# Performance work log

Measured on AMD Instinct MI355X. Metric: run time of the kernel, lower is better.

Reference implementation:

```python
import jax, jax.numpy as jnp
import numpy as np

N_NODES = 50000
N_EDGES = 800000
D = 64
N_REL = 16


def setup_inputs() -> dict:
    key = jax.random.key(0)
    ks = jax.random.split(key, 8)
    return {
        "nfeat": jax.random.normal(ks[0], (N_NODES, D), dtype=jnp.float32),
        "efeat": jax.random.normal(ks[1], (N_EDGES, D), dtype=jnp.float32),
        "relation_W": jax.random.normal(ks[2], (N_REL, D, D), dtype=jnp.float32) * (1.0 / np.sqrt(D)),
        "W1": jax.random.normal(ks[3], (D, D), dtype=jnp.float32) * (1.0 / np.sqrt(D)),
        "W2": jax.random.normal(ks[4], (D, D), dtype=jnp.float32) * (1.0 / np.sqrt(D)),
        "src": jax.random.randint(ks[5], (N_EDGES,), 0, N_NODES, dtype=jnp.int32),
        "dst": jax.random.randint(ks[6], (N_EDGES,), 0, N_NODES, dtype=jnp.int32),
        "etype": jax.random.randint(ks[7], (N_EDGES,), 0, N_REL, dtype=jnp.int32),
    }


def _leaky_relu(x, slope=0.01):
    return jnp.where(x >= 0, x, slope * x)


def reference(nfeat, efeat, relation_W, W1, W2, src, dst, etype):
    N, Din = nfeat.shape
    R, _, Dr = relation_W.shape
    # W_r h for every (relation, node) pair, then gather per-edge.
    # Mathematically identical to per-edge bmm_maybe_select, but avoids the
    # (E, Din, Dr) per-edge weight materialization.
    proj = jnp.einsum('nd,rde->rne', nfeat, relation_W).reshape(R * N, Dr)  # (R*N, Dr)
    flat_src = etype * N + src
    flat_dst = etype * N + dst
    t_r = proj[flat_src]  # (E, Dr) == W_r h_t
    h_r = proj[flat_dst]  # (E, Dr) == W_r h_h
    # att = (W_r h_t)^T tanh(W_r h_h + e_r)
    att = jnp.sum(t_r * jnp.tanh(h_r + efeat), axis=-1)  # (E,)
    # edge softmax grouped by destination node
    seg_max = jax.ops.segment_max(att, dst, num_segments=N)  # (N,)
    ex = jnp.exp(att - seg_max[dst])
    denom = jax.ops.segment_sum(ex, dst, num_segments=N)  # (N,)
    a = ex / denom[dst]  # (E,)
    # u_mul_e + sum scatter aggregation
    h_neighbor = jax.ops.segment_sum(nfeat[src] * a[:, None], dst, num_segments=N)  # (N, Din)
    # Bi-interaction residual
    out = _leaky_relu((nfeat + h_neighbor) @ W1) + _leaky_relu((nfeat * h_neighbor) @ W2)
    return (h_neighbor, out)
```

## Files before the change

### kernel.cpp

```cpp
#include <hip/hip_runtime.h>
#include <math.h>


#define DIM 64
#define PA 72

typedef _Float16 half8 __attribute__((ext_vector_type(8)));
typedef float f32x4 __attribute__((ext_vector_type(4)));

__device__ __forceinline__ float4 f4zero() { return make_float4(0.f, 0.f, 0.f, 0.f); }

__device__ __forceinline__ float fast_tanh(float x) {
    float ex = __expf(2.0f * x);
    return 1.0f - 2.0f / (ex + 1.0f);
}

__global__ __launch_bounds__(256) void k_hist(const int* __restrict__ dst,
                                              int* __restrict__ deg,
                                              int* __restrict__ rank, int E) {
    int e = blockIdx.x * 256 + threadIdx.x;
    if (e < E) rank[e] = atomicAdd(&deg[dst[e]], 1);
}

__global__ __launch_bounds__(256) void k_scan1(const int* __restrict__ deg,
                                               int* __restrict__ epart,
                                               int* __restrict__ bsum, int N) {
    __shared__ int sh[256];
    int i = blockIdx.x * 256 + threadIdx.x;
    int t = threadIdx.x;
    int v = (i < N) ? deg[i] : 0;
    sh[t] = v;
    __syncthreads();
#pragma unroll
    for (int d = 1; d < 256; d <<= 1) {
        int o = (t >= d) ? sh[t - d] : 0;
        __syncthreads();
        sh[t] += o;
        __syncthreads();
    }
    if (i < N) epart[i] = sh[t] - v;
    if (t == 255) bsum[blockIdx.x] = sh[255];
}

__global__ __launch_bounds__(1024) void k_scan2(const int* __restrict__ epart,
                                                const int* __restrict__ bsum,
                                                int nb,
                                                int* __restrict__ off,
                                                int N, int E) {
    __shared__ int bx[256];
    int t = threadIdx.x;
    int v = 0;
    if (t < 256) {
        v = (t < nb) ? bsum[t] : 0;
        bx[t] = v;
    }
    __syncthreads();
#pragma unroll
    for (int d = 1; d < 256; d <<= 1) {
        int o = 0;
        if (t < 256 && t >= d) o = bx[t - d];
        __syncthreads();
        if (t < 256) bx[t] += o;
        __syncthreads();
    }
    if (t < 256) bx[t] -= v;
    __syncthreads();
    for (int i = t; i < N; i += 1024)
        off[i] = epart[i] + bx[i >> 8];
    if (t == 0) off[N] = E;
}

__global__ __launch_bounds__(256) void k_thist(const int* __restrict__ etype,
                                               int* __restrict__ bh,
                                               int nbe, int E) {
    __shared__ int h[16];
    const int tx = threadIdx.x, b = blockIdx.x;
    if (tx < 16) h[tx] = 0;
    __syncthreads();
    int e = b * 256 + tx;
    if (e < E) atomicAdd(&h[etype[e]], 1);
    __syncthreads();
    if (tx < 16) bh[(size_t)tx * nbe + b] = h[tx];
}

__global__ __launch_bounds__(1024) void k_tscan(int* __restrict__ bh, int nbe,
                                                int* __restrict__ hdr) {
    __shared__ int cntS[16];
    __shared__ int tstartS[16];
    const int tx = threadIdx.x;
    const int w = tx >> 6;
    const int lane = tx & 63;
    int* row = bh + (size_t)w * nbe;

    int run = 0;
    for (int i0 = 0; i0 < nbe; i0 += 64) {
        int idx = i0 + lane;
        int v = (idx < nbe) ? row[idx] : 0;
        int incl = v;
#pragma unroll
        for (int d = 1; d < 64; d <<= 1) {
            int o = __shfl_up(incl, d);
            if (lane >= d) incl += o;
        }
        if (idx < nbe) row[idx] = run + (incl - v);
        run += __shfl(incl, 63);
    }
    if (lane == 0) cntS[w] = run;
    __syncthreads();
    if (tx == 0) {
        int ts = 0, tp = 0;
        for (int r = 0; r < 16; ++r) {
            tstartS[r] = ts;
            hdr[r] = ts;
            hdr[17 + r] = tp;
            ts += cntS[r];
            tp += (cntS[r] + 63) >> 6;
        }
        hdr[16] = ts;
        hdr[33] = tp;
    }
    __syncthreads();
    const int t0 = tstartS[w];
    for (int i0 = 0; i0 < nbe; i0 += 64) {
        int idx = i0 + lane;
        if (idx < nbe) row[idx] += t0;
    }
}

__global__ __launch_bounds__(256) void k_tfill(const int* __restrict__ src,
                                               const int* __restrict__ dst,
                                               const int* __restrict__ etype,
                                               const int* __restrict__ rank,
                                               const int* __restrict__ off,
                                               const int* __restrict__ bh, int nbe,
                                               int* __restrict__ sS,
                                               int* __restrict__ dS,
                                               int* __restrict__ pS,
                                               int* __restrict__ eS, int E) {
    __shared__ int h[16];
    const int tx = threadIdx.x, b = blockIdx.x;
    if (tx < 16) h[tx] = 0;
    __syncthreads();
    int e = b * 256 + tx;
    if (e < E) {
        int r = etype[e];
        int mr = atomicAdd(&h[r], 1);
        int slot = bh[(size_t)r * nbe + b] + mr;
        int d = dst[e];
        sS[slot] = src[e];
        dS[slot] = d;
        pS[slot] = off[d] + rank[e];
        eS[slot] = e;
    }
}

__global__ __launch_bounds__(256) void k_attE(const float* __restrict__ nfeat,
                                              const float* __restrict__ efeat,
                                              const float* __restrict__ relW,
                                              const int* __restrict__ hdr,
                                              const int* __restrict__ sS,
                                              const int* __restrict__ dS,
                                              const int* __restrict__ pS,
                                              const int* __restrict__ eS,
                                              float* __restrict__ att_s,
                                              int* __restrict__ src_s) {
    __shared__ _Float16 shS[64 * PA];
    __shared__ _Float16 shD[64 * PA];
    __shared__ _Float16 shB[64 * PA];

    const int bid = blockIdx.x;
    if (bid >= hdr[33]) return;
    int r = 0;
    while (r < 15 && bid >= hdr[17 + r + 1]) ++r;
    const int e0 = hdr[r] + ((bid - hdr[17 + r]) << 6);
    const int cnt = min(64, hdr[r + 1] - e0);

    const int tx = threadIdx.x;

    const float4* Wr4 = (const float4*)(relW + (size_t)r * DIM * DIM);
#pragma unroll
    for (int i = 0; i < 4; ++i) {
        int idx = tx + 256 * i;
        int d = idx >> 4, c = (idx & 15) * 4;
        float4 v = Wr4[idx];
        shB[(c + 0) * PA + d] = (_Float16)v.x;
        shB[(c + 1) * PA + d] = (_Float16)v.y;
        shB[(c + 2) * PA + d] = (_Float16)v.z;
        shB[(c + 3) * PA + d] = (_Float16)v.w;
    }
#pragma unroll
    for (int i = 0; i < 4; ++i) {
        int idx = tx + 256 * i;
        int row = idx >> 4, c = idx & 15;
        bool ok = (row < cnt);
        int sn = ok ? sS[e0 + row] : 0;
        int dn = ok ? dS[e0 + row] : 0;
        float4 a = ok ? *(const float4*)&nfeat[(size_t)sn * DIM + c * 4] : f4zero();
        float4 b = ok ? *(const float4*)&nfeat[(size_t)dn * DIM + c * 4] : f4zero();
        _Float16* p1 = &shS[row * PA + c * 4];
        _Float16* p2 = &shD[row * PA + c * 4];
        p1[0] = (_Float16)a.x; p1[1] = (_Float16)a.y;
        p1[2] = (_Float16)a.z; p1[3] = (_Float16)a.w;
        p2[0] = (_Float16)b.x; p2[1] = (_Float16)b.y;
        p2[2] = (_Float16)b.z; p2[3] = (_Float16)b.w;
    }
    __syncthreads();

    const int w = tx >> 6;
    const int lane = tx & 63;
    const int lm = lane & 15;
    const int lq = lane >> 4;
    const int m0 = w * 16;

    half8 as0 = *(const half8*)&shS[(m0 + lm) * PA + 0 * 32 + lq * 8];
    half8 as1 = *(const half8*)&shS[(m0 + lm) * PA + 1 * 32 + lq * 8];
    half8 ad0 = *(const half8*)&shD[(m0 + lm) * PA + 0 * 32 + lq * 8];
    half8 ad1 = *(const half8*)&shD[(m0 + lm) * PA + 1 * 32 + lq * 8];

    f32x4 T[4], H[4];
#pragma unroll
    for (int ct = 0; ct < 4; ++ct) {
        half8 b0 = *(const half8*)&shB[(ct * 16 + lm) * PA + 0 * 32 + lq * 8];
        half8 b1 = *(const half8*)&shB[(ct * 16 + lm) * PA + 1 * 32 + lq * 8];
        f32x4 c1 = {0.f, 0.f, 0.f, 0.f};
        f32x4 c2 = {0.f, 0.f, 0.f, 0.f};
        c1 = __builtin_amdgcn_mfma_f32_16x16x32_f16(as0, b0, c1, 0, 0, 0);
        c1 = __builtin_amdgcn_mfma_f32_16x16x32_f16(as1, b1, c1, 0, 0, 0);
        c2 = __builtin_amdgcn_mfma_f32_16x16x32_f16(ad0, b0, c2, 0, 0, 0);
        c2 = __builtin_amdgcn_mfma_f32_16x16x32_f16(ad1, b1, c2, 0, 0, 0);
        T[ct] = c1;
        H[ct] = c2;
    }

    int ei[4];
#pragma unroll
    for (int i = 0; i < 4; ++i) {
        int row = m0 + lq * 4 + i;
        ei[i] = (row < cnt) ? eS[e0 + row] : -1;
    }

    float part[4] = {0.f, 0.f, 0.f, 0.f};
#pragma unroll
    for (int ct = 0; ct < 4; ++ct) {
        int col = ct * 16 + lm;
#pragma unroll
        for (int i = 0; i < 4; ++i) {
            float ef = (ei[i] >= 0)
                ? __builtin_nontemporal_load(&efeat[(size_t)ei[i] * DIM + col])
                : 0.f;
            part[i] = fmaf(T[ct][i], fast_tanh(H[ct][i] + ef), part[i]);
        }
    }
#pragma unroll
    for (int i = 0; i < 4; ++i) {
        part[i] += __shfl_xor(part[i], 1);
        part[i] += __shfl_xor(part[i], 2);
        part[i] += __shfl_xor(part[i], 4);
        part[i] += __shfl_xor(part[i], 8);
    }
    if (lm == 0) {
#pragma unroll
        for (int i = 0; i < 4; ++i) {
            int row = m0 + lq * 4 + i;
            if (row < cnt) {
                int p = pS[e0 + row];
                att_s[p] = part[i];
                src_s[p] = sS[e0 + row];
            }
        }
    }
}

__global__ __launch_bounds__(256) void k_agg(const float* __restrict__ att_s,
                                             const int* __restrict__ src_s,
                                             const float* __restrict__ nfeat,
                                             const int* __restrict__ off,
                                             float* __restrict__ hn, int N) {
    const int node = blockIdx.x * 4 + (threadIdx.x >> 6);
    if (node >= N) return;
    const int lane = threadIdx.x & 63;
    const int qw = lane >> 4;
    const int ql = lane & 15;

    const int jb = off[node];
    const int je = off[node + 1];

    float m = -INFINITY;
    for (int j0 = jb; j0 < je; j0 += 64) {
        int j = j0 + lane;
        float a = (j < je) ? att_s[j] : -INFINITY;
        m = fmaxf(m, a);
    }
#pragma unroll
    for (int ms = 32; ms; ms >>= 1) m = fmaxf(m, __shfl_xor(m, ms));

    float pl = 0.f;
    f32x4 acc = {0.f, 0.f, 0.f, 0.f};
    for (int j0 = jb; j0 < je; j0 += 64) {
        int j = j0 + lane;
        int cnt = min(64, je - j0);
        float a = (j < je) ? att_s[j] : -INFINITY;
        float p = __expf(a - m);
        int s = (j < je) ? src_s[j] : 0;
        pl += p;

        int jj = 0;
        for (; jj + 15 < cnt; jj += 16) {
            float pj[4]; int sj[4]; f32x4 x[4];
#pragma unroll
            for (int u = 0; u < 4; ++u) {
                int eidx = jj + u * 4 + qw;
                pj[u] = __shfl(p, eidx);
                sj[u] = __shfl(s, eidx);
            }
#pragma unroll
            for (int u = 0; u < 4; ++u)
                x[u] = *(const f32x4*)&nfeat[(size_t)sj[u] * DIM + ql * 4];
#pragma unroll
            for (int u = 0; u < 4; ++u) {
                acc[0] = fmaf(pj[u], x[u][0], acc[0]);
                acc[1] = fmaf(pj[u], x[u][1], acc[1]);
                acc[2] = fmaf(pj[u], x[u][2], acc[2]);
                acc[3] = fmaf(pj[u], x[u][3], acc[3]);
            }
        }
        for (; jj < cnt; jj += 4) {
            int eidx = jj + qw;
            int ec = (eidx < cnt) ? eidx : (cnt - 1);
            float pj = __shfl(p, ec);
            int sj = __shfl(s, ec);
            if (eidx < cnt) {
                f32x4 x = *(const f32x4*)&nfeat[(size_t)sj * DIM + ql * 4];
                acc[0] = fmaf(pj, x[0], acc[0]);
                acc[1] = fmaf(pj, x[1], acc[1]);
                acc[2] = fmaf(pj, x[2], acc[2]);
                acc[3] = fmaf(pj, x[3], acc[3]);
            }
        }
    }
#pragma unroll
    for (int ms = 32; ms; ms >>= 1) pl += __shfl_xor(pl, ms);

#pragma unroll
    for (int c = 0; c < 4; ++c) {
        acc[c] += __shfl_xor(acc[c], 16);
        acc[c] += __shfl_xor(acc[c], 32);
    }

    const float inv = (je > jb) ? 1.0f / pl : 0.f;
    if (qw == 0) {
        f32x4 hv = {acc[0] * inv, acc[1] * inv, acc[2] * inv, acc[3] * inv};
        *(f32x4*)&hn[(size_t)node * DIM + ql * 4] = hv;
    }
}

__global__ __launch_bounds__(256) void k_bi(const float* __restrict__ nfeat,
                                            const float* __restrict__ hn,
                                            const float* __restrict__ W1,
                                            const float* __restrict__ W2,
                                            float* __restrict__ out, int N) {
    __shared__ _Float16 shMem[4 * 64 * PA];
    _Float16* shA1 = shMem;
    _Float16* shA2 = shMem + 64 * PA;
    _Float16* shB1 = shMem + 2 * 64 * PA;
    _Float16* shB2 = shMem + 3 * 64 * PA;

    const int tx = threadIdx.x;
    const int n0 = blockIdx.x * 64;

    const float4* nf4 = (const float4*)(nfeat + (size_t)n0 * DIM);
    const float4* hn4 = (const float4*)(hn + (size_t)n0 * DIM);
#pragma unroll
    for (int i = 0; i < 4; ++i) {
        int idx = tx + 256 * i;
        int row = idx >> 4, c = idx & 15;
        bool ok = (n0 + row < N);
        float4 a = ok ? nf4[idx] : f4zero();
        float4 b = ok ? hn4[idx] : f4zero();
        _Float16* p1 = &shA1[row * PA + c * 4];
        _Float16* p2 = &shA2[row * PA + c * 4];
        p1[0] = (_Float16)(a.x + b.x); p2[0] = (_Float16)(a.x * b.x);
        p1[1] = (_Float16)(a.y + b.y); p2[1] = (_Float16)(a.y * b.y);
        p1[2] = (_Float16)(a.z + b.z); p2[2] = (_Float16)(a.z * b.z);
        p1[3] = (_Float16)(a.w + b.w); p2[3] = (_Float16)(a.w * b.w);
    }
    const float4* w14 = (const float4*)W1;
    const float4* w24 = (const float4*)W2;
#pragma unroll
    for (int i = 0; i < 4; ++i) {
        int idx = tx + 256 * i;
        int k = idx >> 4, c = (idx & 15) * 4;
        float4 v = w14[idx];
        shB1[(c + 0) * PA + k] = (_Float16)v.x;
        shB1[(c + 1) * PA + k] = (_Float16)v.y;
        shB1[(c + 2) * PA + k] = (_Float16)v.z;
        shB1[(c + 3) * PA + k] = (_Float16)v.w;
        float4 u = w24[idx];
        shB2[(c + 0) * PA + k] = (_Float16)u.x;
        shB2[(c + 1) * PA + k] = (_Float16)u.y;
        shB2[(c + 2) * PA + k] = (_Float16)u.z;
        shB2[(c + 3) * PA + k] = (_Float16)u.w;
    }
    __syncthreads();

    const int w = tx >> 6;
    const int lane = tx & 63;
    const int lm = lane & 15;
    const int lq = lane >> 4;
    const int m0 = w * 16;

    half8 a10 = *(const half8*)&shA1[(m0 + lm) * PA + 0 * 32 + lq * 8];
    half8 a11 = *(const half8*)&shA1[(m0 + lm) * PA + 1 * 32 + lq * 8];
    half8 a20 = *(const half8*)&shA2[(m0 + lm) * PA + 0 * 32 + lq * 8];
    half8 a21 = *(const half8*)&shA2[(m0 + lm) * PA + 1 * 32 + lq * 8];

    f32x4 res[4];
#pragma unroll
    for (int ct = 0; ct < 4; ++ct) {
        half8 b10 = *(const half8*)&shB1[(ct * 16 + lm) * PA + 0 * 32 + lq * 8];
        half8 b11 = *(const half8*)&shB1[(ct * 16 + lm) * PA + 1 * 32 + lq * 8];
        half8 b20 = *(const half8*)&shB2[(ct * 16 + lm) * PA + 0 * 32 + lq * 8];
        half8 b21 = *(const half8*)&shB2[(ct * 16 + lm) * PA + 1 * 32 + lq * 8];
        f32x4 c1 = {0.f, 0.f, 0.f, 0.f};
        f32x4 c2 = {0.f, 0.f, 0.f, 0.f};
        c1 = __builtin_amdgcn_mfma_f32_16x16x32_f16(a10, b10, c1, 0, 0, 0);
        c1 = __builtin_amdgcn_mfma_f32_16x16x32_f16(a11, b11, c1, 0, 0, 0);
        c2 = __builtin_amdgcn_mfma_f32_16x16x32_f16(a20, b20, c2, 0, 0, 0);
        c2 = __builtin_amdgcn_mfma_f32_16x16x32_f16(a21, b21, c2, 0, 0, 0);
#pragma unroll
        for (int i = 0; i < 4; ++i) {
            float o1 = c1[i], o2 = c2[i];
            res[ct][i] = (o1 >= 0.f ? o1 : 0.01f * o1) + (o2 >= 0.f ? o2 : 0.01f * o2);
        }
    }

    __syncthreads();
    float* shSt = (float*)shMem;
#pragma unroll
    for (int ct = 0; ct < 4; ++ct)
#pragma unroll
        for (int i = 0; i < 4; ++i)
            shSt[(m0 + lq * 4 + i) * 68 + ct * 16 + lm] = res[ct][i];
    __syncthreads();

    float* outp = out + (size_t)n0 * DIM;
#pragma unroll
    for (int k = 0; k < 4; ++k) {
        int idx = tx + 256 * k;
        int row = idx >> 4, cc = idx & 15;
        if (n0 + row < N) {
            float4 v = *(const float4*)&shSt[row * 68 + cc * 4];
            *(float4*)&outp[(size_t)row * DIM + cc * 4] = v;
        }
    }
}

extern "C" void kernel_launch(void* const* d_in, const int* in_sizes, int n_in,
                              void* d_out, int out_size, void* d_ws, size_t ws_size,
                              hipStream_t stream) {
    const float* nfeat = (const float*)d_in[0];
    const float* efeat = (const float*)d_in[1];
    const float* relW  = (const float*)d_in[2];
    const float* W1    = (const float*)d_in[3];
    const float* W2    = (const float*)d_in[4];
    const int* src   = (const int*)d_in[5];
    const int* dst   = (const int*)d_in[6];
    const int* etype = (const int*)d_in[7];

    const int N = in_sizes[0] / DIM;
    const int E = in_sizes[5];
    const int NB = (N + 255) / 256;
    const int NBE = (E + 255) / 256;

    float* out = (float*)d_out;
    float* hn  = out;
    float* bi  = out + (size_t)N * DIM;

    int* deg    = (int*)d_ws;
    int* off    = deg + N;
    int* epart  = off + (N + 1);
    int* bsum   = epart + N;
    int* rank   = bsum + 256;
    int* src_s  = rank + E;
    float* att_s = (float*)(src_s + E);
    int* bh     = (int*)(att_s + E);
    int* hdr    = bh + (size_t)16 * NBE;
    int* sS     = hdr + 64;
    int* dS     = sS + E;
    int* pS     = dS + E;
    int* eS     = pS + E;

    (void)hipMemsetAsync(deg, 0, (size_t)N * sizeof(int), stream);

    k_hist<<<NBE, 256, 0, stream>>>(dst, deg, rank, E);
    k_scan1<<<NB, 256, 0, stream>>>(deg, epart, bsum, N);
    k_scan2<<<1, 1024, 0, stream>>>(epart, bsum, NB, off, N, E);

    k_thist<<<NBE, 256, 0, stream>>>(etype, bh, NBE, E);
    k_tscan<<<1, 1024, 0, stream>>>(bh, NBE, hdr);
    k_tfill<<<NBE, 256, 0, stream>>>(src, dst, etype, rank, off, bh, NBE,
                                     sS, dS, pS, eS, E);

    const int nTiles = (E + 63) / 64 + 16;
    k_attE<<<nTiles, 256, 0, stream>>>(nfeat, efeat, relW, hdr,
                                       sS, dS, pS, eS, att_s, src_s);

    k_agg<<<(N + 3) / 4, 256, 0, stream>>>(att_s, src_s, nfeat, off, hn, N);

    k_bi<<<(N + 63) / 64, 256, 0, stream>>>(nfeat, hn, W1, W2, bi, N);
}
```

Measured before the change: 548.4 us.

## Fuse preprocessing kernels, pretranspose relation weights, stage efeat rows through LDS

Merges the degree histogram and the per-block etype histogram into one kernel, which also converts the relation weights once into a transposed fp16 buffer. The two single-block scans are merged into one launch. The attention kernel now reads the prepared fp16 weights straight into registers instead of rebuilding them in LDS in every tile. It also loads efeat rows coalesced into shared memory as float4 instead of scattered scalar loads per MFMA output. This removes two launches and redundant per-tile weight conversion, at the cost of extra syncs and LDS reuse in the attention kernel.

```diff
diff --git a/kernel.cpp b/kernel.cpp
--- a/kernel.cpp
+++ b/kernel.cpp
@@ -6,6 +6,7 @@
 #define PA 72
 
 typedef _Float16 half8 __attribute__((ext_vector_type(8)));
+typedef _Float16 half4 __attribute__((ext_vector_type(4)));
 typedef float f32x4 __attribute__((ext_vector_type(4)));
 
 __device__ __forceinline__ float4 f4zero() { return make_float4(0.f, 0.f, 0.f, 0.f); }
@@ -15,11 +16,40 @@
     return 1.0f - 2.0f / (ex + 1.0f);
 }
 
-__global__ __launch_bounds__(256) void k_hist(const int* __restrict__ dst,
-                                              int* __restrict__ deg,
-                                              int* __restrict__ rank, int E) {
-    int e = blockIdx.x * 256 + threadIdx.x;
-    if (e < E) rank[e] = atomicAdd(&deg[dst[e]], 1);
+__global__ __launch_bounds__(256) void k_histT(const int* __restrict__ dst,
+                                               const int* __restrict__ etype,
+                                               const float* __restrict__ relW,
+                                               int* __restrict__ deg,
+                                               int* __restrict__ rank,
+                                               int* __restrict__ bh,
+                                               _Float16* __restrict__ WT,
+                                               int nbe, int E) {
+    __shared__ int h[16];
+    const int tx = threadIdx.x, b = blockIdx.x;
+    if (tx < 16) h[tx] = 0;
+    __syncthreads();
+    int e = b * 256 + tx;
+    if (e < E) {
+        rank[e] = atomicAdd(&deg[dst[e]], 1);
+        atomicAdd(&h[etype[e]], 1);
+    }
+    __syncthreads();
+    if (tx < 16) bh[(size_t)tx * nbe + b] = h[tx];
+
+    if (b < 16) {
+        const float4* Wr4 = (const float4*)(relW + (size_t)b * DIM * DIM);
+        _Float16* wt = WT + (size_t)b * DIM * DIM;
+#pragma unroll
+        for (int i = 0; i < 4; ++i) {
+            int idx = tx + 256 * i;
+            int k = idx >> 4, c4 = (idx & 15) * 4;
+            float4 v = Wr4[idx];
+            wt[(c4 + 0) * DIM + k] = (_Float16)v.x;
+            wt[(c4 + 1) * DIM + k] = (_Float16)v.y;
+            wt[(c4 + 2) * DIM + k] = (_Float16)v.z;
+            wt[(c4 + 3) * DIM + k] = (_Float16)v.w;
+        }
+    }
 }
 
 __global__ __launch_bounds__(256) void k_scan1(const int* __restrict__ deg,
@@ -42,70 +72,37 @@
     if (t == 255) bsum[blockIdx.x] = sh[255];
 }
 
-__global__ __launch_bounds__(1024) void k_scan2(const int* __restrict__ epart,
+__global__ __launch_bounds__(1024) void k_scanF(int* __restrict__ bh, int nbe,
+                                                int* __restrict__ hdr,
+                                                const int* __restrict__ epart,
                                                 const int* __restrict__ bsum,
                                                 int nb,
                                                 int* __restrict__ off,
                                                 int N, int E) {
-    __shared__ int bx[256];
-    int t = threadIdx.x;
-    int v = 0;
-    if (t < 256) {
-        v = (t < nb) ? bsum[t] : 0;
-        bx[t] = v;
-    }
-    __syncthreads();
-#pragma unroll
-    for (int d = 1; d < 256; d <<= 1) {
-        int o = 0;
-        if (t < 256 && t >= d) o = bx[t - d];
-        __syncthreads();
-        if (t < 256) bx[t] += o;
-        __syncthreads();
-    }
-    if (t < 256) bx[t] -= v;
-    __syncthreads();
-    for (int i = t; i < N; i += 1024)
-        off[i] = epart[i] + bx[i >> 8];
-    if (t == 0) off[N] = E;
-}
-
-__global__ __launch_bounds__(256) void k_thist(const int* __restrict__ etype,
-                                               int* __restrict__ bh,
-                                               int nbe, int E) {
-    __shared__ int h[16];
-    const int tx = threadIdx.x, b = blockIdx.x;
-    if (tx < 16) h[tx] = 0;
-    __syncthreads();
-    int e = b * 256 + tx;
-    if (e < E) atomicAdd(&h[etype[e]], 1);
-    __syncthreads();
-    if (tx < 16) bh[(size_t)tx * nbe + b] = h[tx];
-}
-
-__global__ __launch_bounds__(1024) void k_tscan(int* __restrict__ bh, int nbe,
-                                                int* __restrict__ hdr) {
     __shared__ int cntS[16];
     __shared__ int tstartS[16];
+    __shared__ int bx[256];
     const int tx = threadIdx.x;
     const int w = tx >> 6;
     const int lane = tx & 63;
-    int* row = bh + (size_t)w * nbe;
-
-    int run = 0;
-    for (int i0 = 0; i0 < nbe; i0 += 64) {
-        int idx = i0 + lane;
-        int v = (idx < nbe) ? row[idx] : 0;
-        int incl = v;
-#pragma unroll
-        for (int d = 1; d < 64; d <<= 1) {
-            int o = __shfl_up(incl, d);
-            if (lane >= d) incl += o;
-        }
-        if (idx < nbe) row[idx] = run + (incl - v);
-        run += __shfl(incl, 63);
-    }
-    if (lane == 0) cntS[w] = run;
+
+    {
+        int* row = bh + (size_t)w * nbe;
+        int run = 0;
+        for (int i0 = 0; i0 < nbe; i0 += 64) {
+            int idx = i0 + lane;
+            int v = (idx < nbe) ? row[idx] : 0;
+            int incl = v;
+#pragma unroll
+            for (int d = 1; d < 64; d <<= 1) {
+                int o = __shfl_up(incl, d);
+                if (lane >= d) incl += o;
+            }
+            if (idx < nbe) row[idx] = run + (incl - v);
+            run += __shfl(incl, 63);
+        }
+        if (lane == 0) cntS[w] = run;
+    }
     __syncthreads();
     if (tx == 0) {
         int ts = 0, tp = 0;
@@ -120,11 +117,33 @@
         hdr[33] = tp;
     }
     __syncthreads();
-    const int t0 = tstartS[w];
-    for (int i0 = 0; i0 < nbe; i0 += 64) {
-        int idx = i0 + lane;
-        if (idx < nbe) row[idx] += t0;
-    }
+    {
+        const int t0 = tstartS[w];
+        int* row = bh + (size_t)w * nbe;
+        for (int i0 = 0; i0 < nbe; i0 += 64) {
+            int idx = i0 + lane;
+            if (idx < nbe) row[idx] += t0;
+        }
+    }
+    int v = 0;
+    if (tx < 256) {
+        v = (tx < nb) ? bsum[tx] : 0;
+        bx[tx] = v;
+    }
+    __syncthreads();
+#pragma unroll
+    for (int d = 1; d < 256; d <<= 1) {
+        int o = 0;
+        if (tx < 256 && tx >= d) o = bx[tx - d];
+        __syncthreads();
+        if (tx < 256) bx[tx] += o;
+        __syncthreads();
+    }
+    if (tx < 256) bx[tx] -= v;
+    __syncthreads();
+    for (int i = tx; i < N; i += 1024)
+        off[i] = epart[i] + bx[i >> 8];
+    if (tx == 0) off[N] = E;
 }
 
 __global__ __launch_bounds__(256) void k_tfill(const int* __restrict__ src,
@@ -156,7 +175,7 @@
 
 __global__ __launch_bounds__(256) void k_attE(const float* __restrict__ nfeat,
                                               const float* __restrict__ efeat,
-                                              const float* __restrict__ relW,
+                                              const _Float16* __restrict__ WT,
                                               const int* __restrict__ hdr,
                                               const int* __restrict__ sS,
                                               const int* __restrict__ dS,
@@ -164,9 +183,9 @@
                                               const int* __restrict__ eS,
                                               float* __restrict__ att_s,
                                               int* __restrict__ src_s) {
-    __shared__ _Float16 shS[64 * PA];
-    __shared__ _Float16 shD[64 * PA];
-    __shared__ _Float16 shB[64 * PA];
+    __shared__ _Float16 shMem[2 * 64 * PA];
+    _Float16* shS = shMem;
+    _Float16* shD = shMem + 64 * PA;
 
     const int bid = blockIdx.x;
     if (bid >= hdr[33]) return;
@@ -174,20 +193,8 @@
     while (r < 15 && bid >= hdr[17 + r + 1]) ++r;
     const int e0 = hdr[r] + ((bid - hdr[17 + r]) << 6);
     const int cnt = min(64, hdr[r + 1] - e0);
-
     const int tx = threadIdx.x;
 
-    const float4* Wr4 = (const float4*)(relW + (size_t)r * DIM * DIM);
-#pragma unroll
-    for (int i = 0; i < 4; ++i) {
-        int idx = tx + 256 * i;
-        int d = idx >> 4, c = (idx & 15) * 4;
-        float4 v = Wr4[idx];
-        shB[(c + 0) * PA + d] = (_Float16)v.x;
-        shB[(c + 1) * PA + d] = (_Float16)v.y;
-        shB[(c + 2) * PA + d] = (_Float16)v.z;
-        shB[(c + 3) * PA + d] = (_Float16)v.w;
-    }
 #pragma unroll
     for (int i = 0; i < 4; ++i) {
         int idx = tx + 256 * i;
@@ -197,12 +204,10 @@
         int dn = ok ? dS[e0 + row] : 0;
         float4 a = ok ? *(const float4*)&nfeat[(size_t)sn * DIM + c * 4] : f4zero();
         float4 b = ok ? *(const float4*)&nfeat[(size_t)dn * DIM + c * 4] : f4zero();
-        _Float16* p1 = &shS[row * PA + c * 4];
-        _Float16* p2 = &shD[row * PA + c * 4];
-        p1[0] = (_Float16)a.x; p1[1] = (_Float16)a.y;
-        p1[2] = (_Float16)a.z; p1[3] = (_Float16)a.w;
-        p2[0] = (_Float16)b.x; p2[1] = (_Float16)b.y;
-        p2[2] = (_Float16)b.z; p2[3] = (_Float16)b.w;
+        half4 ha = {(_Float16)a.x, (_Float16)a.y, (_Float16)a.z, (_Float16)a.w};
+        half4 hb = {(_Float16)b.x, (_Float16)b.y, (_Float16)b.z, (_Float16)b.w};
+        *(half4*)&shS[row * PA + c * 4] = ha;
+        *(half4*)&shD[row * PA + c * 4] = hb;
     }
     __syncthreads();
 
@@ -212,32 +217,46 @@
     const int lq = lane >> 4;
     const int m0 = w * 16;
 
-    half8 as0 = *(const half8*)&shS[(m0 + lm) * PA + 0 * 32 + lq * 8];
-    half8 as1 = *(const half8*)&shS[(m0 + lm) * PA + 1 * 32 + lq * 8];
-    half8 ad0 = *(const half8*)&shD[(m0 + lm) * PA + 0 * 32 + lq * 8];
-    half8 ad1 = *(const half8*)&shD[(m0 + lm) * PA + 1 * 32 + lq * 8];
+    half8 as0 = *(const half8*)&shS[(m0 + lm) * PA + lq * 8];
+    half8 as1 = *(const half8*)&shS[(m0 + lm) * PA + 32 + lq * 8];
+    half8 ad0 = *(const half8*)&shD[(m0 + lm) * PA + lq * 8];
+    half8 ad1 = *(const half8*)&shD[(m0 + lm) * PA + 32 + lq * 8];
+
+    const _Float16* wt = WT + (size_t)r * DIM * DIM;
+    half8 b0[4], b1[4];
+#pragma unroll
+    for (int ct = 0; ct < 4; ++ct) {
+        b0[ct] = *(const half8*)&wt[(ct * 16 + lm) * DIM + lq * 8];
+        b1[ct] = *(const half8*)&wt[(ct * 16 + lm) * DIM + 32 + lq * 8];
+    }
+    __syncthreads();
+
+    float* shE = (float*)shMem;
+#pragma unroll
+    for (int i = 0; i < 4; ++i) {
+        int idx = tx + 256 * i;
+        int row = idx >> 4, c = idx & 15;
+        if (row < cnt) {
+            int e = eS[e0 + row];
+            f32x4 v = __builtin_nontemporal_load(
+                (const f32x4*)&efeat[(size_t)e * DIM + c * 4]);
+            *(f32x4*)&shE[row * 68 + c * 4] = v;
+        }
+    }
 
     f32x4 T[4], H[4];
 #pragma unroll
     for (int ct = 0; ct < 4; ++ct) {
-        half8 b0 = *(const half8*)&shB[(ct * 16 + lm) * PA + 0 * 32 + lq * 8];
-        half8 b1 = *(const half8*)&shB[(ct * 16 + lm) * PA + 1 * 32 + lq * 8];
         f32x4 c1 = {0.f, 0.f, 0.f, 0.f};
         f32x4 c2 = {0.f, 0.f, 0.f, 0.f};
-        c1 = __builtin_amdgcn_mfma_f32_16x16x32_f16(as0, b0, c1, 0, 0, 0);
-        c1 = __builtin_amdgcn_mfma_f32_16x16x32_f16(as1, b1, c1, 0, 0, 0);
-        c2 = __builtin_amdgcn_mfma_f32_16x16x32_f16(ad0, b0, c2, 0, 0, 0);
-        c2 = __builtin_amdgcn_mfma_f32_16x16x32_f16(ad1, b1, c2, 0, 0, 0);
+        c1 = __builtin_amdgcn_mfma_f32_16x16x32_f16(as0, b0[ct], c1, 0, 0, 0);
+        c1 = __builtin_amdgcn_mfma_f32_16x16x32_f16(as1, b1[ct], c1, 0, 0, 0);
+        c2 = __builtin_amdgcn_mfma_f32_16x16x32_f16(ad0, b0[ct], c2, 0, 0, 0);
+        c2 = __builtin_amdgcn_mfma_f32_16x16x32_f16(ad1, b1[ct], c2, 0, 0, 0);
         T[ct] = c1;
         H[ct] = c2;
     }
-
-    int ei[4];
-#pragma unroll
-    for (int i = 0; i < 4; ++i) {
-        int row = m0 + lq * 4 + i;
-        ei[i] = (row < cnt) ? eS[e0 + row] : -1;
-    }
+    __syncthreads();
 
     float part[4] = {0.f, 0.f, 0.f, 0.f};
 #pragma unroll
@@ -245,9 +264,8 @@
         int col = ct * 16 + lm;
 #pragma unroll
         for (int i = 0; i < 4; ++i) {
-            float ef = (ei[i] >= 0)
-                ? __builtin_nontemporal_load(&efeat[(size_t)ei[i] * DIM + col])
-                : 0.f;
+            int row = m0 + lq * 4 + i;
+            float ef = shE[row * 68 + col];
             part[i] = fmaf(T[ct][i], fast_tanh(H[ct][i] + ef), part[i]);
         }
     }
@@ -409,18 +427,18 @@
     const int lq = lane >> 4;
     const int m0 = w * 16;
 
-    half8 a10 = *(const half8*)&shA1[(m0 + lm) * PA + 0 * 32 + lq * 8];
-    half8 a11 = *(const half8*)&shA1[(m0 + lm) * PA + 1 * 32 + lq * 8];
-    half8 a20 = *(const half8*)&shA2[(m0 + lm) * PA + 0 * 32 + lq * 8];
-    half8 a21 = *(const half8*)&shA2[(m0 + lm) * PA + 1 * 32 + lq * 8];
+    half8 a10 = *(const half8*)&shA1[(m0 + lm) * PA + lq * 8];
+    half8 a11 = *(const half8*)&shA1[(m0 + lm) * PA + 32 + lq * 8];
+    half8 a20 = *(const half8*)&shA2[(m0 + lm) * PA + lq * 8];
+    half8 a21 = *(const half8*)&shA2[(m0 + lm) * PA + 32 + lq * 8];
 
     f32x4 res[4];
 #pragma unroll
     for (int ct = 0; ct < 4; ++ct) {
-        half8 b10 = *(const half8*)&shB1[(ct * 16 + lm) * PA + 0 * 32 + lq * 8];
-        half8 b11 = *(const half8*)&shB1[(ct * 16 + lm) * PA + 1 * 32 + lq * 8];
-        half8 b20 = *(const half8*)&shB2[(ct * 16 + lm) * PA + 0 * 32 + lq * 8];
-        half8 b21 = *(const half8*)&shB2[(ct * 16 + lm) * PA + 1 * 32 + lq * 8];
+        half8 b10 = *(const half8*)&shB1[(ct * 16 + lm) * PA + lq * 8];
+        half8 b11 = *(const half8*)&shB1[(ct * 16 + lm) * PA + 32 + lq * 8];
+        half8 b20 = *(const half8*)&shB2[(ct * 16 + lm) * PA + lq * 8];
+        half8 b21 = *(const half8*)&shB2[(ct * 16 + lm) * PA + 32 + lq * 8];
         f32x4 c1 = {0.f, 0.f, 0.f, 0.f};
         f32x4 c2 = {0.f, 0.f, 0.f, 0.f};
         c1 = __builtin_amdgcn_mfma_f32_16x16x32_f16(a10, b10, c1, 0, 0, 0);
@@ -489,20 +507,18 @@
     int* dS     = sS + E;
     int* pS     = dS + E;
     int* eS     = pS + E;
+    _Float16* WT = (_Float16*)(eS + E);
 
     (void)hipMemsetAsync(deg, 0, (size_t)N * sizeof(int), stream);
 
-    k_hist<<<NBE, 256, 0, stream>>>(dst, deg, rank, E);
+    k_histT<<<NBE, 256, 0, stream>>>(dst, etype, relW, deg, rank, bh, WT, NBE, E);
     k_scan1<<<NB, 256, 0, stream>>>(deg, epart, bsum, N);
-    k_scan2<<<1, 1024, 0, stream>>>(epart, bsum, NB, off, N, E);
-
-    k_thist<<<NBE, 256, 0, stream>>>(etype, bh, NBE, E);
-    k_tscan<<<1, 1024, 0, stream>>>(bh, NBE, hdr);
+    k_scanF<<<1, 1024, 0, stream>>>(bh, NBE, hdr, epart, bsum, NB, off, N, E);
     k_tfill<<<NBE, 256, 0, stream>>>(src, dst, etype, rank, off, bh, NBE,
                                      sS, dS, pS, eS, E);
 
     const int nTiles = (E + 63) / 64 + 16;
-    k_attE<<<nTiles, 256, 0, stream>>>(nfeat, efeat, relW, hdr,
+    k_attE<<<nTiles, 256, 0, stream>>>(nfeat, efeat, WT, hdr,
                                        sS, dS, pS, eS, att_s, src_s);
 
     k_agg<<<(N + 3) / 4, 256, 0, stream>>>(att_s, src_s, nfeat, off, hn, N);
```

After: 586.9 us. 7.0% more time.
